# Performance work log

Measured on AMD Instinct MI355X. Metric: run time of the kernel, lower is better.

Reference implementation:

```python
import jax, jax.numpy as jnp
import numpy as np

VOCAB = 200000
EMB = 128
HID = 128
NT = 16
B = 4096


def setup_inputs() -> dict:
    key = jax.random.key(0)
    ks = jax.random.split(key, 8)
    x = jax.random.randint(ks[0], (B, 1), 0, VOCAB, dtype=jnp.int64)
    emb = jax.random.normal(ks[1], (VOCAB, EMB), dtype=jnp.float32) * 0.02
    emb = emb.at[0].set(0.0)  # padding_idx=0
    s = 1.0 / np.sqrt(HID)
    w_ih = jax.random.uniform(ks[2], (4 * HID, EMB), minval=-s, maxval=s, dtype=jnp.float32)
    w_hh = jax.random.uniform(ks[3], (4 * HID, HID), minval=-s, maxval=s, dtype=jnp.float32)
    b_ih = jax.random.uniform(ks[4], (4 * HID,), minval=-s, maxval=s, dtype=jnp.float32)
    b_hh = jax.random.uniform(ks[5], (4 * HID,), minval=-s, maxval=s, dtype=jnp.float32)
    w_fc = jax.random.uniform(ks[6], (NT, HID), minval=-s, maxval=s, dtype=jnp.float32)
    b_fc = jax.random.uniform(ks[7], (NT,), minval=-s, maxval=s, dtype=jnp.float32)
    return {"x": x, "emb": emb, "w_ih": w_ih, "w_hh": w_hh,
            "b_ih": b_ih, "b_hh": b_hh, "w_fc": w_fc, "b_fc": b_fc}


def _lstm(xs, w_ih, w_hh, b_ih, b_hh):
    # xs: [T, E]; torch LSTM with batch=1, gate order i, f, g, o
    H = HID
    b = b_ih + b_hh

    def step(carry, xt):
        h, c = carry
        z = xt @ w_ih.T + h @ w_hh.T + b  # [4H]
        i = jax.nn.sigmoid(z[:H])
        f = jax.nn.sigmoid(z[H:2 * H])
        g = jnp.tanh(z[2 * H:3 * H])
        o = jax.nn.sigmoid(z[3 * H:])
        c = f * c + i * g
        h = o * jnp.tanh(c)
        return (h, c), h

    init = (jnp.zeros((H,), xs.dtype), jnp.zeros((H,), xs.dtype))
    _, hs = jax.lax.scan(step, init, xs)
    return hs  # [T, H]


def reference(x, emb, w_ih, w_hh, b_ih, b_hh, w_fc, b_fc):
    emb = emb.at[0].set(0.0)  # padding_idx=0
    xe = emb[x[:, 0]]  # [B, E] == lstm input viewed as (seq=B, batch=1, E)
    hs = _lstm(xe, w_ih, w_hh, b_ih, b_hh)  # [B, H]
    out = hs @ w_fc.T + b_fc  # [B, NT]; torch .squeeze(1) is a no-op for NT>1
    return out
```

## Files before the change

kernel.cpp:

```cpp
#include <hip/hip_runtime.h>
#include <math.h>

#define EMBD 128
#define HIDD 128
#define NTAR 16
#define BSEQ 4096
#define G4   512
#define CH   8

typedef float v2f __attribute__((ext_vector_type(2)));

#define DPP_ADD(x, ctrl)                                                     \
    ((x) + __int_as_float(__builtin_amdgcn_update_dpp(                       \
               0, __float_as_int(x), (ctrl), 0xf, 0xf, true)))

__device__ __forceinline__ float fast_sigmoid(float z) {
    return __builtin_amdgcn_rcpf(1.f + __expf(-z));
}
__device__ __forceinline__ float fast_tanh(float z) {
    return 1.f - 2.f * __builtin_amdgcn_rcpf(1.f + __expf(2.f * z));
}

__global__ void input_proj_kernel(const int* __restrict__ x,
                                  const float* __restrict__ emb,
                                  const float* __restrict__ w_ih,
                                  const float* __restrict__ b_ih,
                                  const float* __restrict__ b_hh,
                                  float* __restrict__ zxT) {
    const int t = blockIdx.x;
    const int j = threadIdx.x;
    const int u = j >> 2;
    const int g = j & 3;
    const int row = g * HIDD + u;
    const int idx = x[t];
    const float4* __restrict__ er = (const float4*)(emb + (long long)idx * EMBD);
    const float4* __restrict__ wr = (const float4*)(w_ih + row * EMBD);
    float acc = 0.f;
#pragma unroll
    for (int k = 0; k < EMBD / 4; ++k) {
        float4 e = er[k];
        float4 w = wr[k];
        acc += e.x * w.x + e.y * w.y + e.z * w.z + e.w * w.w;
    }
    zxT[(t * HIDD + u) * 4 + g] = acc + b_ih[row] + b_hh[row];
}

__global__ __launch_bounds__(512, 2)
void lstm_seq_kernel(const float* __restrict__ zxT,
                     const float* __restrict__ w_hh,
                     float* __restrict__ hs) {
    __shared__ float h_db[2][HIDD];

    const int tid = threadIdx.x;
    const int l   = tid & 63;
    const int wv  = tid >> 6;
    const int kq  = l & 3;
    const int us  = l >> 2;
    const int u   = wv * 16 + us;
    const bool writer = (kq == 0);

    v2f w2[4][16];
#pragma unroll
    for (int g = 0; g < 4; ++g) {
        const float* __restrict__ wr = w_hh + (g * HIDD + u) * HIDD;
#pragma unroll
        for (int k4 = 0; k4 < 8; ++k4) {
            const int c0 = 32 * kq + ((4 * k4 + 8 * kq) & 31);
            float4 v = *(const float4*)(wr + c0);
            w2[g][2 * k4 + 0] = (v2f){v.x, v.y};
            w2[g][2 * k4 + 1] = (v2f){v.z, v.w};
        }
    }
#pragma unroll
    for (int g = 0; g < 4; ++g)
#pragma unroll
        for (int k = 0; k < 16; ++k)
            asm volatile("" : "+v"(w2[g][k]));

    if (tid < HIDD) { h_db[0][tid] = 0.f; h_db[1][tid] = 0.f; }
    float c = 0.f;
    float hreg[CH];
    float4 zcur[CH];
#pragma unroll
    for (int s = 0; s < CH; ++s) hreg[s] = 0.f;

    const float4* __restrict__ zx4 = (const float4*)zxT;
    __syncthreads();

    for (int tc = 0; tc < BSEQ; tc += CH) {
        if (writer && tc > 0) {
#pragma unroll
            for (int s = 0; s < CH; ++s)
                hs[(tc - CH + s) * HIDD + u] = hreg[s];
        }
#pragma unroll
        for (int s = 0; s < CH; ++s)
            zcur[s] = zx4[(tc + s) * HIDD + u];

#pragma unroll
        for (int s = 0; s < CH; ++s) {
            const float* __restrict__ rb = h_db[s & 1];
            const int    wb             = (s & 1) ^ 1;

            float4 hv[8];
#pragma unroll
            for (int k4 = 0; k4 < 8; ++k4) {
                const int c0 = 32 * kq + ((4 * k4 + 8 * kq) & 31);
                hv[k4] = *(const float4*)(rb + c0);
            }

            v2f a[4] = {(v2f){0.f,0.f},(v2f){0.f,0.f},(v2f){0.f,0.f},(v2f){0.f,0.f}};
#pragma unroll
            for (int k4 = 0; k4 < 8; ++k4) {
                const v2f hlo = (v2f){hv[k4].x, hv[k4].y};
                const v2f hhi = (v2f){hv[k4].z, hv[k4].w};
#pragma unroll
                for (int g = 0; g < 4; ++g) {
                    a[g] += hlo * w2[g][2 * k4 + 0];
                    a[g] += hhi * w2[g][2 * k4 + 1];
                }
            }

            float z0 = a[0].x + a[0].y, z1 = a[1].x + a[1].y;
            float z2 = a[2].x + a[2].y, z3 = a[3].x + a[3].y;
            z0 = DPP_ADD(z0, 0xB1); z0 = DPP_ADD(z0, 0x4E);
            z1 = DPP_ADD(z1, 0xB1); z1 = DPP_ADD(z1, 0x4E);
            z2 = DPP_ADD(z2, 0xB1); z2 = DPP_ADD(z2, 0x4E);
            z3 = DPP_ADD(z3, 0xB1); z3 = DPP_ADD(z3, 0x4E);

            const float4 zb = zcur[s];
            const float gi = fast_sigmoid(z0 + zb.x);
            const float gf = fast_sigmoid(z1 + zb.y);
            const float gg = fast_tanh   (z2 + zb.z);
            const float go = fast_sigmoid(z3 + zb.w);
            c = gf * c + gi * gg;
            const float h = go * fast_tanh(c);
            hreg[s] = h;
            if (writer) h_db[wb][u] = h;
            __syncthreads();
        }
    }
    if (writer) {
#pragma unroll
        for (int s = 0; s < CH; ++s)
            hs[(BSEQ - CH + s) * HIDD + u] = hreg[s];
    }
}

__global__ void fc_kernel(const float* __restrict__ hs,
                          const float* __restrict__ w_fc,
                          const float* __restrict__ b_fc,
                          float* __restrict__ out) {
    const int gid = blockIdx.x * blockDim.x + threadIdx.x;
    if (gid >= BSEQ * NTAR) return;
    const int n = gid & (NTAR - 1);
    const int t = gid >> 4;
    const float4* __restrict__ hr = (const float4*)(hs + t * HIDD);
    const float4* __restrict__ wr = (const float4*)(w_fc + n * HIDD);
    float acc = 0.f;
#pragma unroll
    for (int k = 0; k < HIDD / 4; ++k) {
        float4 h = hr[k];
        float4 wv = wr[k];
        acc += h.x * wv.x + h.y * wv.y + h.z * wv.z + h.w * wv.w;
    }
    out[gid] = acc + b_fc[n];
}

extern "C" void kernel_launch(void* const* d_in, const int* in_sizes, int n_in,
                              void* d_out, int out_size, void* d_ws, size_t ws_size,
                              hipStream_t stream) {
    const int*   x    = (const int*)d_in[0];
    const float* emb  = (const float*)d_in[1];
    const float* w_ih = (const float*)d_in[2];
    const float* w_hh = (const float*)d_in[3];
    const float* b_ih = (const float*)d_in[4];
    const float* b_hh = (const float*)d_in[5];
    const float* w_fc = (const float*)d_in[6];
    const float* b_fc = (const float*)d_in[7];
    float* out = (float*)d_out;

    float* zxT = (float*)d_ws;
    float* hs  = zxT + (size_t)BSEQ * G4;

    input_proj_kernel<<<BSEQ, G4, 0, stream>>>(x, emb, w_ih, b_ih, b_hh, zxT);
    lstm_seq_kernel<<<1, 512, 0, stream>>>(zxT, w_hh, hs);
    fc_kernel<<<(BSEQ * NTAR + 255) / 256, 256, 0, stream>>>(hs, w_fc, b_fc, out);
}
```

Measured before the change: 2.536 ms.

## Use fp16 MFMA for recurrent matvec and prefetch next input-projection chunk

The per-step h·W_hh matvec in the sequential LSTM kernel now runs on 16x16x32 fp16 MFMA instructions instead of packed fp32 FMAs with DPP reductions. W_hh is held in registers as fp16 and the hidden state is kept in shared memory as fp16. Only one row of the A matrix carries h; the other rows read a zero pad. The next chunk's input projections are loaded one chunk ahead to hide global-load latency. The aim is a shorter latency per serial step, at the cost of fp16 rounding of weights and h that compounds over 4096 steps, plus MFMA pipeline latency on a mostly empty 16-row matrix.

Result: faster. 2.096 ms (-17.3%).

```diff
diff --git a/kernel.cpp b/kernel.cpp
--- a/kernel.cpp
+++ b/kernel.cpp
@@ -8,11 +8,8 @@
 #define G4   512
 #define CH   8
 
-typedef float v2f __attribute__((ext_vector_type(2)));
-
-#define DPP_ADD(x, ctrl)                                                     \
-    ((x) + __int_as_float(__builtin_amdgcn_update_dpp(                       \
-               0, __float_as_int(x), (ctrl), 0xf, 0xf, true)))
+typedef _Float16 v8h __attribute__((ext_vector_type(8)));
+typedef float    v4f __attribute__((ext_vector_type(4)));
 
 __device__ __forceinline__ float fast_sigmoid(float z) {
     return __builtin_amdgcn_rcpf(1.f + __expf(-z));
@@ -49,98 +46,116 @@
 void lstm_seq_kernel(const float* __restrict__ zxT,
                      const float* __restrict__ w_hh,
                      float* __restrict__ hs) {
-    __shared__ float h_db[2][HIDD];
+    __shared__ __align__(16) _Float16 h_db[2][HIDD];
+    __shared__ __align__(16) _Float16 zpad[8];
 
     const int tid = threadIdx.x;
     const int l   = tid & 63;
     const int wv  = tid >> 6;
-    const int kq  = l & 3;
-    const int us  = l >> 2;
-    const int u   = wv * 16 + us;
-    const bool writer = (kq == 0);
-
-    v2f w2[4][16];
+    const int n   = l & 15;
+    const int qd  = l >> 4;
+    const int U0  = wv * 16;
+    const int u   = U0 + n;
+    const bool lane16 = (l < 16);
+
+    v8h b[4][4];
 #pragma unroll
     for (int g = 0; g < 4; ++g) {
-        const float* __restrict__ wr = w_hh + (g * HIDD + u) * HIDD;
-#pragma unroll
-        for (int k4 = 0; k4 < 8; ++k4) {
-            const int c0 = 32 * kq + ((4 * k4 + 8 * kq) & 31);
-            float4 v = *(const float4*)(wr + c0);
-            w2[g][2 * k4 + 0] = (v2f){v.x, v.y};
-            w2[g][2 * k4 + 1] = (v2f){v.z, v.w};
+#pragma unroll
+        for (int q = 0; q < 4; ++q) {
+            const float* __restrict__ wr =
+                w_hh + (g * HIDD + u) * HIDD + q * 32 + qd * 8;
+            v8h f;
+#pragma unroll
+            for (int j = 0; j < 8; ++j) f[j] = (_Float16)wr[j];
+            b[g][q] = f;
         }
     }
 #pragma unroll
     for (int g = 0; g < 4; ++g)
 #pragma unroll
-        for (int k = 0; k < 16; ++k)
-            asm volatile("" : "+v"(w2[g][k]));
-
-    if (tid < HIDD) { h_db[0][tid] = 0.f; h_db[1][tid] = 0.f; }
+        for (int q = 0; q < 4; ++q)
+            asm volatile("" : "+v"(b[g][q]));
+
+    if (tid < HIDD) { h_db[0][tid] = (_Float16)0.f; h_db[1][tid] = (_Float16)0.f; }
+    if (tid < 8)    zpad[tid] = (_Float16)0.f;
+
+    const bool leader = (n == 0);
+    const _Float16* abase0 = leader ? &h_db[0][qd * 8] : &zpad[0];
+    const _Float16* abase1 = leader ? &h_db[1][qd * 8] : &zpad[0];
+    const int astep = leader ? 32 : 0;
+
     float c = 0.f;
     float hreg[CH];
-    float4 zcur[CH];
-#pragma unroll
-    for (int s = 0; s < CH; ++s) hreg[s] = 0.f;
-
+    float4 zcur[CH], zfut[CH];
     const float4* __restrict__ zx4 = (const float4*)zxT;
+#pragma unroll
+    for (int s = 0; s < CH; ++s) {
+        zcur[s] = zx4[s * HIDD + u];
+        hreg[s] = 0.f;
+    }
     __syncthreads();
 
     for (int tc = 0; tc < BSEQ; tc += CH) {
-        if (writer && tc > 0) {
+        if (lane16 && tc > 0) {
 #pragma unroll
             for (int s = 0; s < CH; ++s)
                 hs[(tc - CH + s) * HIDD + u] = hreg[s];
         }
-#pragma unroll
-        for (int s = 0; s < CH; ++s)
-            zcur[s] = zx4[(tc + s) * HIDD + u];
+        {
+            const int tn = (tc + CH < BSEQ) ? (tc + CH) : (BSEQ - CH);
+#pragma unroll
+            for (int s = 0; s < CH; ++s)
+                zfut[s] = zx4[(tn + s) * HIDD + u];
+        }
 
 #pragma unroll
         for (int s = 0; s < CH; ++s) {
-            const float* __restrict__ rb = h_db[s & 1];
-            const int    wb             = (s & 1) ^ 1;
-
-            float4 hv[8];
-#pragma unroll
-            for (int k4 = 0; k4 < 8; ++k4) {
-                const int c0 = 32 * kq + ((4 * k4 + 8 * kq) & 31);
-                hv[k4] = *(const float4*)(rb + c0);
-            }
-
-            v2f a[4] = {(v2f){0.f,0.f},(v2f){0.f,0.f},(v2f){0.f,0.f},(v2f){0.f,0.f}};
-#pragma unroll
-            for (int k4 = 0; k4 < 8; ++k4) {
-                const v2f hlo = (v2f){hv[k4].x, hv[k4].y};
-                const v2f hhi = (v2f){hv[k4].z, hv[k4].w};
-#pragma unroll
-                for (int g = 0; g < 4; ++g) {
-                    a[g] += hlo * w2[g][2 * k4 + 0];
-                    a[g] += hhi * w2[g][2 * k4 + 1];
-                }
-            }
-
-            float z0 = a[0].x + a[0].y, z1 = a[1].x + a[1].y;
-            float z2 = a[2].x + a[2].y, z3 = a[3].x + a[3].y;
-            z0 = DPP_ADD(z0, 0xB1); z0 = DPP_ADD(z0, 0x4E);
-            z1 = DPP_ADD(z1, 0xB1); z1 = DPP_ADD(z1, 0x4E);
-            z2 = DPP_ADD(z2, 0xB1); z2 = DPP_ADD(z2, 0x4E);
-            z3 = DPP_ADD(z3, 0xB1); z3 = DPP_ADD(z3, 0x4E);
+            const _Float16* ab = (s & 1) ? abase1 : abase0;
+            const int wb = (s & 1) ^ 1;
+
+            v8h a0 = *(const v8h*)(ab + 0 * astep);
+            v8h a1 = *(const v8h*)(ab + 1 * astep);
+            v8h a2 = *(const v8h*)(ab + 2 * astep);
+            v8h a3 = *(const v8h*)(ab + 3 * astep);
+
+            v4f d0 = {0.f, 0.f, 0.f, 0.f}, d1 = d0, d2 = d0, d3 = d0;
+            d0 = __builtin_amdgcn_mfma_f32_16x16x32_f16(a0, b[0][0], d0, 0, 0, 0);
+            d1 = __builtin_amdgcn_mfma_f32_16x16x32_f16(a0, b[1][0], d1, 0, 0, 0);
+            d2 = __builtin_amdgcn_mfma_f32_16x16x32_f16(a0, b[2][0], d2, 0, 0, 0);
+            d3 = __builtin_amdgcn_mfma_f32_16x16x32_f16(a0, b[3][0], d3, 0, 0, 0);
+            d0 = __builtin_amdgcn_mfma_f32_16x16x32_f16(a1, b[0][1], d0, 0, 0, 0);
+            d1 = __builtin_amdgcn_mfma_f32_16x16x32_f16(a1, b[1][1], d1, 0, 0, 0);
+            d2 = __builtin_amdgcn_mfma_f32_16x16x32_f16(a1, b[2][1], d2, 0, 0, 0);
+            d3 = __builtin_amdgcn_mfma_f32_16x16x32_f16(a1, b[3][1], d3, 0, 0, 0);
+            d0 = __builtin_amdgcn_mfma_f32_16x16x32_f16(a2, b[0][2], d0, 0, 0, 0);
+            d1 = __builtin_amdgcn_mfma_f32_16x16x32_f16(a2, b[1][2], d1, 0, 0, 0);
+            d2 = __builtin_amdgcn_mfma_f32_16x16x32_f16(a2, b[2][2], d2, 0, 0, 0);
+            d3 = __builtin_amdgcn_mfma_f32_16x16x32_f16(a2, b[3][2], d3, 0, 0, 0);
+            d0 = __builtin_amdgcn_mfma_f32_16x16x32_f16(a3, b[0][3], d0, 0, 0, 0);
+            d1 = __builtin_amdgcn_mfma_f32_16x16x32_f16(a3, b[1][3], d1, 0, 0, 0);
+            d2 = __builtin_amdgcn_mfma_f32_16x16x32_f16(a3, b[2][3], d2, 0, 0, 0);
+            d3 = __builtin_amdgcn_mfma_f32_16x16x32_f16(a3, b[3][3], d3, 0, 0, 0);
 
             const float4 zb = zcur[s];
-            const float gi = fast_sigmoid(z0 + zb.x);
-            const float gf = fast_sigmoid(z1 + zb.y);
-            const float gg = fast_tanh   (z2 + zb.z);
-            const float go = fast_sigmoid(z3 + zb.w);
+            const float zi = d0[0] + zb.x;
+            const float zf = d1[0] + zb.y;
+            const float zg = d2[0] + zb.z;
+            const float zo = d3[0] + zb.w;
+            const float gi = fast_sigmoid(zi);
+            const float gf = fast_sigmoid(zf);
+            const float gg = fast_tanh(zg);
+            const float go = fast_sigmoid(zo);
             c = gf * c + gi * gg;
             const float h = go * fast_tanh(c);
             hreg[s] = h;
-            if (writer) h_db[wb][u] = h;
+            if (lane16) h_db[wb][u] = (_Float16)h;
             __syncthreads();
         }
-    }
-    if (writer) {
+#pragma unroll
+        for (int s = 0; s < CH; ++s) zcur[s] = zfut[s];
+    }
+    if (lane16) {
 #pragma unroll
         for (int s = 0; s < CH; ++s)
             hs[(BSEQ - CH + s) * HIDD + u] = hreg[s];
```
